# Performance work log

Measured on AMD Instinct MI355X. Metric: run time of the kernel, lower is better.

The kernel has to match this reference:

```python
import jax, jax.numpy as jnp
import numpy as np

B, C, H, W = 8, 64, 256, 256  # H must equal W (matmul shape constraint in original)


def setup_inputs() -> dict:
    key = jax.random.key(0)
    ks = jax.random.split(key, 7)
    s = 1.0 / np.sqrt(C)  # fan-in scaled init, like conv default scale
    return {
        "x": jax.random.normal(ks[0], (B, C, H, W), dtype=jnp.float32),
        "Wq": jax.random.normal(ks[1], (C, C), dtype=jnp.float32) * s,
        "bq": jax.random.normal(ks[2], (C,), dtype=jnp.float32) * s,
        "Wk": jax.random.normal(ks[3], (C, C), dtype=jnp.float32) * s,
        "bk": jax.random.normal(ks[4], (C,), dtype=jnp.float32) * s,
        "Wv": jax.random.normal(ks[5], (C, C), dtype=jnp.float32) * s,
        "bv": jax.random.normal(ks[6], (C,), dtype=jnp.float32) * s,
    }


def _conv1x1(x, Wt, b):
    # 1x1 Conv2d == per-pixel GEMM over channels: [o,c] x [b,c,h,w] -> [b,o,h,w]
    return jnp.einsum("oc,bchw->bohw", Wt, x) + b[None, :, None, None]


def reference(x, Wq, bq, Wk, bk, Wv, bv):
    q = _conv1x1(x, Wq, bq)
    k = _conv1x1(x, Wk, bk)
    v = _conv1x1(x, Wv, bv)
    # attn[b,c,i,j] = sum_h q[b,c,h,i] * k[b,c,h,j]   (q^T @ k over spatial)
    attn = jnp.einsum("bchi,bchj->bcij", q, k)
    # softmax over the CHANNEL axis (dim=-3 in torch == axis 1 here)
    attn = jax.nn.softmax(attn, axis=1)
    # out[b,c,i,j] = sum_m attn[b,c,i,m] * v[b,c,m,j]  (requires H == W)
    out = jnp.einsum("bcim,bcmj->bcij", attn, v)
    return out
```

## Files before the change

kernel.cpp:

```cpp
#include <hip/hip_runtime.h>
#include <math.h>

constexpr int CH  = 64;
constexpr int WW  = 256;
constexpr int HWS = WW * WW;
constexpr int NB  = 8;

typedef __attribute__((ext_vector_type(8))) short bf16x8;
typedef __attribute__((ext_vector_type(4))) float f32x4;

__device__ inline ushort f2bf(float f) {
    uint u = __float_as_uint(f);
    u += 0x7fffu + ((u >> 16) & 1u);
    return (ushort)(u >> 16);
}

union FragU { uint u[4]; bf16x8 v; };

__global__ __launch_bounds__(256) void qkv_mfma(
    const float* __restrict__ x,
    const float* __restrict__ Wq, const float* __restrict__ bq,
    const float* __restrict__ Wk, const float* __restrict__ bk,
    const float* __restrict__ Wv, const float* __restrict__ bv,
    float* __restrict__ Q, float* __restrict__ K, ushort* __restrict__ V)
{
    __shared__ ushort Xhi[128 * 64] __attribute__((aligned(16)));
    __shared__ ushort Xlo[128 * 64] __attribute__((aligned(16)));

    const int tid  = threadIdx.x;
    const int ln   = tid & 63;
    const int wid  = tid >> 6;
    const int ml   = ln & 15;
    const int quad = ln >> 4;

    const int n0 = blockIdx.x * 128;
    const int b  = n0 >> 16;
    const int pb = n0 & 65535;
    const float* xb = x + ((size_t)(b * CH) << 16);

    bf16x8 Ah[3][2], Al[3][2];
    float biasv[3][4];
#pragma unroll
    for (int a = 0; a < 3; ++a) {
        const int mt = wid * 3 + a;
        const float* Wsrc = (mt < 4) ? Wq : (mt < 8) ? Wk : Wv;
        const float* bsrc = (mt < 4) ? bq : (mt < 8) ? bk : bv;
        const int o = (mt & 3) * 16 + ml;
#pragma unroll
        for (int kf = 0; kf < 2; ++kf) {
            FragU Hh, Ll;
#pragma unroll
            for (int rp = 0; rp < 4; ++rp) {
                const float f0 = Wsrc[o * 64 + kf * 32 + quad * 8 + rp * 2];
                const float f1 = Wsrc[o * 64 + kf * 32 + quad * 8 + rp * 2 + 1];
                const uint u0 = __float_as_uint(f0);
                const uint u1 = __float_as_uint(f1);
                const float g0 = f0 - __uint_as_float(u0 & 0xffff0000u);
                const float g1 = f1 - __uint_as_float(u1 & 0xffff0000u);
                Hh.u[rp] = __builtin_amdgcn_perm(u1, u0, 0x07060302u);
                Ll.u[rp] = __builtin_amdgcn_perm(__float_as_uint(g1),
                                                 __float_as_uint(g0), 0x07060302u);
            }
            Ah[a][kf] = Hh.v; Al[a][kf] = Ll.v;
        }
#pragma unroll
        for (int r = 0; r < 4; ++r)
            biasv[a][r] = bsrc[(mt & 3) * 16 + quad * 4 + r];
    }

#pragma unroll
    for (int p = 0; p < 8; ++p) {
        const int flat = p * 256 + tid;
        const int c    = flat >> 5;
        const int px4  = (flat & 31) * 4;
        const float4 xv = *(const float4*)&xb[((size_t)c << 16) + pb + px4];
#pragma unroll
        for (int u = 0; u < 4; ++u) {
            const int px = px4 + u;
            const float f = (&xv.x)[u];
            const uint fu = __float_as_uint(f);
            const float lo = f - __uint_as_float(fu & 0xffff0000u);
            const int adr = px * 64 + ((((c >> 3) ^ ((px >> 1) & 7))) << 3) + (c & 7);
            Xhi[adr] = (ushort)(fu >> 16);
            Xlo[adr] = (ushort)(__float_as_uint(lo) >> 16);
        }
    }
    __syncthreads();

    f32x4 acc[3][8];
    const f32x4 zero = {0.f, 0.f, 0.f, 0.f};
#pragma unroll
    for (int a = 0; a < 3; ++a)
#pragma unroll
        for (int t = 0; t < 8; ++t) acc[a][t] = zero;

#pragma unroll
    for (int t = 0; t < 8; ++t) {
        const int px = t * 16 + ml;
        bf16x8 Bh[2], Bl[2];
#pragma unroll
        for (int kf = 0; kf < 2; ++kf) {
            const int g   = kf * 4 + quad;
            const int adr = px * 64 + ((g ^ ((px >> 1) & 7)) << 3);
            Bh[kf] = *(const bf16x8*)&Xhi[adr];
            Bl[kf] = *(const bf16x8*)&Xlo[adr];
        }
#pragma unroll
        for (int a = 0; a < 3; ++a) {
#pragma unroll
            for (int kf = 0; kf < 2; ++kf) {
                acc[a][t] = __builtin_amdgcn_mfma_f32_16x16x32_bf16(Ah[a][kf], Bh[kf], acc[a][t], 0, 0, 0);
                acc[a][t] = __builtin_amdgcn_mfma_f32_16x16x32_bf16(Ah[a][kf], Bl[kf], acc[a][t], 0, 0, 0);
                acc[a][t] = __builtin_amdgcn_mfma_f32_16x16x32_bf16(Al[a][kf], Bh[kf], acc[a][t], 0, 0, 0);
            }
        }
    }

#pragma unroll
    for (int a = 0; a < 3; ++a) {
        const int mt = wid * 3 + a;
        const int ch = (mt & 3) * 16 + quad * 4;
        if (mt < 4) {
#pragma unroll
            for (int t = 0; t < 8; ++t)
#pragma unroll
                for (int r = 0; r < 4; ++r)
                    Q[((size_t)(b * CH + ch + r) << 16) + pb + t * 16 + ml] =
                        acc[a][t][r] + biasv[a][r];
        } else if (mt < 8) {
#pragma unroll
            for (int t = 0; t < 8; ++t)
#pragma unroll
                for (int r = 0; r < 4; ++r)
                    K[((size_t)(b * CH + ch + r) << 16) + pb + t * 16 + ml] =
                        acc[a][t][r] + biasv[a][r];
        } else {
#pragma unroll
            for (int t = 0; t < 8; ++t)
#pragma unroll
                for (int r = 0; r < 4; ++r)
                    V[((size_t)(b * CH + ch + r) << 16) + pb + t * 16 + ml] =
                        f2bf(acc[a][t][r] + biasv[a][r]);
        }
    }
}

__device__ inline void frag_split(const float* __restrict__ S, int col, int quad,
                                  bf16x8* hi, bf16x8* lo) {
    FragU H, L;
#pragma unroll
    for (int rp = 0; rp < 4; ++rp) {
        const int h0 = quad * 8 + rp * 2;
        const int sw = ((h0 >> 1) & 7) << 2;
        const int c  = col ^ sw;
        const float f0 = S[(h0    ) * 128 + c];
        const float f1 = S[(h0 + 1) * 128 + c];
        const uint u0 = __float_as_uint(f0);
        const uint u1 = __float_as_uint(f1);
        const float g0 = f0 - __uint_as_float(u0 & 0xffff0000u);
        const float g1 = f1 - __uint_as_float(u1 & 0xffff0000u);
        H.u[rp] = __builtin_amdgcn_perm(u1, u0, 0x07060302u);
        L.u[rp] = __builtin_amdgcn_perm(__float_as_uint(g1), __float_as_uint(g0),
                                        0x07060302u);
    }
    *hi = H.v; *lo = L.v;
}

__global__ __launch_bounds__(256, 3) void attn_mfma(
    const float* __restrict__ Q, const float* __restrict__ Kt,
    float* __restrict__ attn)
{
    const int gid = blockIdx.x;
    const int bc  = gid >> 2;
    const int i0  = ((gid >> 1) & 1) * 128;
    const int j0  = (gid & 1) * 128;
    const float* q = Q  + (size_t)bc * HWS;
    const float* k = Kt + (size_t)bc * HWS;
    float* out     = attn + (size_t)bc * HWS;

    __shared__ float As[32 * 128];
    __shared__ float Bs[32 * 128];

    const int tid  = threadIdx.x;
    const int L    = tid & 63;
    const int wid  = tid >> 6;
    const int wy   = (wid >> 1) * 64;
    const int wx   = (wid & 1) * 64;
    const int ml   = L & 15;
    const int quad = L >> 4;

    f32x4 zero = {0.f, 0.f, 0.f, 0.f};
    f32x4 acc[4][4];
#pragma unroll
    for (int a = 0; a < 4; ++a)
#pragma unroll
        for (int b = 0; b < 4; ++b) acc[a][b] = zero;

    for (int k0 = 0; k0 < WW; k0 += 32) {
#pragma unroll
        for (int p = 0; p < 4; ++p) {
            const int flat = p * 256 + tid;
            const int hh   = flat >> 5;
            const int i4   = (flat & 31) * 4;
            const int sw   = ((hh >> 1) & 7) << 2;
            *(float4*)&As[hh * 128 + (i4 ^ sw)] =
                *(const float4*)&q[(size_t)(k0 + hh) * WW + i0 + i4];
            *(float4*)&Bs[hh * 128 + (i4 ^ sw)] =
                *(const float4*)&k[(size_t)(k0 + hh) * WW + j0 + i4];
        }
        __syncthreads();

        bf16x8 bh[4], bl[4];
#pragma unroll
        for (int t = 0; t < 4; ++t)
            frag_split(Bs, wx + t * 16 + ml, quad, &bh[t], &bl[t]);
#pragma unroll
        for (int a = 0; a < 4; ++a) {
            bf16x8 ah, al;
            frag_split(As, wy + a * 16 + ml, quad, &ah, &al);
#pragma unroll
            for (int b = 0; b < 4; ++b) {
                acc[a][b] = __builtin_amdgcn_mfma_f32_16x16x32_bf16(ah, bh[b], acc[a][b], 0, 0, 0);
                acc[a][b] = __builtin_amdgcn_mfma_f32_16x16x32_bf16(ah, bl[b], acc[a][b], 0, 0, 0);
                acc[a][b] = __builtin_amdgcn_mfma_f32_16x16x32_bf16(al, bh[b], acc[a][b], 0, 0, 0);
            }
        }
        __syncthreads();
    }

#pragma unroll
    for (int a = 0; a < 4; ++a)
#pragma unroll
        for (int b = 0; b < 4; ++b)
#pragma unroll
            for (int r = 0; r < 4; ++r)
                out[(size_t)(i0 + wy + a * 16 + quad * 4 + r) * WW
                    + j0 + wx + b * 16 + ml] = acc[a][b][r];
}

__global__ __launch_bounds__(256) void transpose_v(
    const ushort* __restrict__ Vb, ushort* __restrict__ Vt)
{
    const int blk = blockIdx.x;
    const int bc  = blk >> 2;
    const int m0  = ((blk >> 1) & 1) * 128;
    const int j0  = (blk & 1) * 128;
    const ushort* src = Vb + (size_t)bc * HWS;
    ushort* dst       = Vt + (size_t)bc * HWS;

    __shared__ ushort T[128][128] __attribute__((aligned(16)));

    const int tid = threadIdx.x;
#pragma unroll
    for (int p = 0; p < 8; ++p) {
        const int id  = p * 256 + tid;
        const int mm  = id >> 4;
        const int c16 = id & 15;
        const int cg  = (c16 + (mm >> 3)) & 15;
        *(uint4*)&T[mm][cg * 8] =
            *(const uint4*)(src + (size_t)(m0 + mm) * WW + j0 + c16 * 8);
    }
    __syncthreads();
#pragma unroll
    for (int p = 0; p < 4; ++p) {
        const int id  = p * 256 + tid;
        const int c16 = id & 15;
        const int jjp = id >> 4;
        const int jj  = jjp * 2;
        const int jjg = jj >> 3;
        ushort ra[8], rb[8];
#pragma unroll
        for (int u = 0; u < 8; ++u) {
            const int mm = c16 * 8 + u;
            const int cg = (jjg + c16) & 15;
            const uint pr = *(const uint*)&T[mm][cg * 8 + (jj & 7)];
            ra[u] = (ushort)(pr & 0xffffu);
            rb[u] = (ushort)(pr >> 16);
        }
        *(uint4*)(dst + (size_t)(j0 + jj)     * WW + m0 + c16 * 8) = *(uint4*)ra;
        *(uint4*)(dst + (size_t)(j0 + jj + 1) * WW + m0 + c16 * 8) = *(uint4*)rb;
    }
}

__global__ __launch_bounds__(128) void softmax_kernel(
    const float* __restrict__ logits, ushort* __restrict__ Wb)
{
    const int gid = blockIdx.x;
    const int b   = gid >> 8;
    const int i   = gid & 255;
    const int j2  = threadIdx.x * 2;
    const size_t off = (((size_t)(b * CH)) << 16) + (size_t)i * WW + j2;
    const float* base = logits + off;
    ushort* wout      = Wb + off;

    float2 v[CH];
#pragma unroll
    for (int c = 0; c < CH; ++c) v[c] = *(const float2*)&base[((size_t)c) << 16];

    float mx = v[0].x, my = v[0].y;
#pragma unroll
    for (int c = 1; c < CH; ++c) { mx = fmaxf(mx, v[c].x); my = fmaxf(my, v[c].y); }

    float sx = 0.f, sy = 0.f;
#pragma unroll
    for (int c = 0; c < CH; ++c) {
        v[c].x = __expf(v[c].x - mx); sx += v[c].x;
        v[c].y = __expf(v[c].y - my); sy += v[c].y;
    }
    const float ix = 1.0f / sx, iy = 1.0f / sy;
#pragma unroll
    for (int c = 0; c < CH; ++c) {
        ushort2 o;
        o.x = f2bf(v[c].x * ix);
        o.y = f2bf(v[c].y * iy);
        *(ushort2*)&wout[((size_t)c) << 16] = o;
    }
}

__global__ __launch_bounds__(256) void pv_kernel2(
    const ushort* __restrict__ Wb, const ushort* __restrict__ Vt,
    float* __restrict__ out)
{
    const int blk = blockIdx.x;
    const int bc  = blk >> 2;
    const int i0  = ((blk >> 1) & 1) * 128;
    const int j0  = (blk & 1) * 128;
    const ushort* w  = Wb + (size_t)bc * HWS;
    const ushort* vt = Vt + (size_t)bc * HWS;
    float* o         = out + (size_t)bc * HWS;

    __shared__ ushort As[128][40] __attribute__((aligned(16)));
    __shared__ ushort Bs[128][40] __attribute__((aligned(16)));

    const int tid  = threadIdx.x;
    const int L    = tid & 63;
    const int wid  = tid >> 6;
    const int wy   = (wid >> 1) * 64;
    const int wx   = (wid & 1) * 64;
    const int ml   = L & 15;
    const int quad = L >> 4;

    f32x4 zero = {0.f, 0.f, 0.f, 0.f};
    f32x4 acc[4][4];
#pragma unroll
    for (int a = 0; a < 4; ++a)
#pragma unroll
        for (int b = 0; b < 4; ++b) acc[a][b] = zero;

    for (int m0 = 0; m0 < WW; m0 += 32) {
#pragma unroll
        for (int p = 0; p < 2; ++p) {
            const int id  = p * 256 + tid;
            const int row = id >> 2;
            const int c4  = id & 3;
            *(uint4*)&As[row][c4 * 8] =
                *(const uint4*)(w  + (size_t)(i0 + row) * WW + m0 + c4 * 8);
            *(uint4*)&Bs[row][c4 * 8] =
                *(const uint4*)(vt + (size_t)(j0 + row) * WW + m0 + c4 * 8);
        }
        __syncthreads();

        bf16x8 af[4], bfr[4];
#pragma unroll
        for (int t = 0; t < 4; ++t)
            af[t]  = *(const bf16x8*)&As[wy + t * 16 + ml][quad * 8];
#pragma unroll
        for (int t = 0; t < 4; ++t)
            bfr[t] = *(const bf16x8*)&Bs[wx + t * 16 + ml][quad * 8];
#pragma unroll
        for (int a = 0; a < 4; ++a)
#pragma unroll
            for (int b = 0; b < 4; ++b)
                acc[a][b] = __builtin_amdgcn_mfma_f32_16x16x32_bf16(
                    af[a], bfr[b], acc[a][b], 0, 0, 0);
        __syncthreads();
    }

#pragma unroll
    for (int a = 0; a < 4; ++a)
#pragma unroll
        for (int b = 0; b < 4; ++b)
#pragma unroll
            for (int r = 0; r < 4; ++r)
                o[(size_t)(i0 + wy + a * 16 + quad * 4 + r) * WW
                  + j0 + wx + b * 16 + ml] = acc[a][b][r];
}

extern "C" void kernel_launch(void* const* d_in, const int* in_sizes, int n_in,
                              void* d_out, int out_size, void* d_ws, size_t ws_size,
                              hipStream_t stream) {
    const float* x  = (const float*)d_in[0];
    const float* Wq = (const float*)d_in[1];
    const float* bq = (const float*)d_in[2];
    const float* Wk = (const float*)d_in[3];
    const float* bk = (const float*)d_in[4];
    const float* Wv = (const float*)d_in[5];
    const float* bv = (const float*)d_in[6];
    float* out = (float*)d_out;

    const size_t NEL = (size_t)NB * CH * HWS;
    float*  Q  = (float*)d_ws;
    float*  K  = Q + NEL;
    ushort* Vb = (ushort*)(K + NEL);
    ushort* Vt = Vb + NEL;
    ushort* Wb = (ushort*)d_ws;

    qkv_mfma<<<(NB * HWS) / 128, 256, 0, stream>>>(x, Wq, bq, Wk, bk, Wv, bv, Q, K, Vb);
    attn_mfma<<<NB * CH * 4, 256, 0, stream>>>(Q, K, out);
    transpose_v<<<NB * CH * 4, 256, 0, stream>>>(Vb, Vt);
    softmax_kernel<<<NB * WW, 128, 0, stream>>>(out, Wb);
    pv_kernel2<<<NB * CH * 4, 256, 0, stream>>>(Wb, Vt, out);
}
```

Baseline: 615.3 us.

## Pre-pack Q/K as bf16 hi/lo pairs and load MFMA fragments directly from global

The QKV projection now stores Q and K as packed 32-bit words holding a bf16 high part and a bf16 residual, so the attention kernel no longer has to do the split arithmetic. The attention kernel drops the LDS staging, the barriers and the per-tile hi/lo split. Each lane gathers its fragment elements straight from global memory with strided scalar loads and assembles the hi and lo fragments with byte perms. This trades LDS traffic and synchronisation for uncoalesced-looking per-lane global loads (rows strided by WW) and more registers, and it removes the occupancy hint of 3 from launch bounds.

```diff
diff --git a/kernel.cpp b/kernel.cpp
--- a/kernel.cpp
+++ b/kernel.cpp
@@ -13,6 +13,12 @@
     uint u = __float_as_uint(f);
     u += 0x7fffu + ((u >> 16) & 1u);
     return (ushort)(u >> 16);
+}
+
+__device__ inline uint packsplit(float f) {
+    const uint fu = __float_as_uint(f);
+    const float lo = f - __uint_as_float(fu & 0xffff0000u);
+    return (fu & 0xffff0000u) | (__float_as_uint(lo) >> 16);
 }
 
 union FragU { uint u[4]; bf16x8 v; };
@@ -22,7 +28,7 @@
     const float* __restrict__ Wq, const float* __restrict__ bq,
     const float* __restrict__ Wk, const float* __restrict__ bk,
     const float* __restrict__ Wv, const float* __restrict__ bv,
-    float* __restrict__ Q, float* __restrict__ K, ushort* __restrict__ V)
+    uint* __restrict__ Q, uint* __restrict__ K, ushort* __restrict__ V)
 {
     __shared__ ushort Xhi[128 * 64] __attribute__((aligned(16)));
     __shared__ ushort Xlo[128 * 64] __attribute__((aligned(16)));
@@ -126,14 +132,14 @@
 #pragma unroll
                 for (int r = 0; r < 4; ++r)
                     Q[((size_t)(b * CH + ch + r) << 16) + pb + t * 16 + ml] =
-                        acc[a][t][r] + biasv[a][r];
+                        packsplit(acc[a][t][r] + biasv[a][r]);
         } else if (mt < 8) {
 #pragma unroll
             for (int t = 0; t < 8; ++t)
 #pragma unroll
                 for (int r = 0; r < 4; ++r)
                     K[((size_t)(b * CH + ch + r) << 16) + pb + t * 16 + ml] =
-                        acc[a][t][r] + biasv[a][r];
+                        packsplit(acc[a][t][r] + biasv[a][r]);
         } else {
 #pragma unroll
             for (int t = 0; t < 8; ++t)
@@ -145,41 +151,17 @@
     }
 }
 
-__device__ inline void frag_split(const float* __restrict__ S, int col, int quad,
-                                  bf16x8* hi, bf16x8* lo) {
-    FragU H, L;
-#pragma unroll
-    for (int rp = 0; rp < 4; ++rp) {
-        const int h0 = quad * 8 + rp * 2;
-        const int sw = ((h0 >> 1) & 7) << 2;
-        const int c  = col ^ sw;
-        const float f0 = S[(h0    ) * 128 + c];
-        const float f1 = S[(h0 + 1) * 128 + c];
-        const uint u0 = __float_as_uint(f0);
-        const uint u1 = __float_as_uint(f1);
-        const float g0 = f0 - __uint_as_float(u0 & 0xffff0000u);
-        const float g1 = f1 - __uint_as_float(u1 & 0xffff0000u);
-        H.u[rp] = __builtin_amdgcn_perm(u1, u0, 0x07060302u);
-        L.u[rp] = __builtin_amdgcn_perm(__float_as_uint(g1), __float_as_uint(g0),
-                                        0x07060302u);
-    }
-    *hi = H.v; *lo = L.v;
-}
-
-__global__ __launch_bounds__(256, 3) void attn_mfma(
-    const float* __restrict__ Q, const float* __restrict__ Kt,
+__global__ __launch_bounds__(256) void attn_mfma2(
+    const uint* __restrict__ Qp, const uint* __restrict__ Kp,
     float* __restrict__ attn)
 {
     const int gid = blockIdx.x;
     const int bc  = gid >> 2;
     const int i0  = ((gid >> 1) & 1) * 128;
     const int j0  = (gid & 1) * 128;
-    const float* q = Q  + (size_t)bc * HWS;
-    const float* k = Kt + (size_t)bc * HWS;
-    float* out     = attn + (size_t)bc * HWS;
-
-    __shared__ float As[32 * 128];
-    __shared__ float Bs[32 * 128];
+    const uint* q = Qp + (size_t)bc * HWS;
+    const uint* k = Kp + (size_t)bc * HWS;
+    float* out    = attn + (size_t)bc * HWS;
 
     const int tid  = threadIdx.x;
     const int L    = tid & 63;
@@ -189,7 +171,7 @@
     const int ml   = L & 15;
     const int quad = L >> 4;
 
-    f32x4 zero = {0.f, 0.f, 0.f, 0.f};
+    const f32x4 zero = {0.f, 0.f, 0.f, 0.f};
     f32x4 acc[4][4];
 #pragma unroll
     for (int a = 0; a < 4; ++a)
@@ -197,35 +179,51 @@
         for (int b = 0; b < 4; ++b) acc[a][b] = zero;
 
     for (int k0 = 0; k0 < WW; k0 += 32) {
-#pragma unroll
-        for (int p = 0; p < 4; ++p) {
-            const int flat = p * 256 + tid;
-            const int hh   = flat >> 5;
-            const int i4   = (flat & 31) * 4;
-            const int sw   = ((hh >> 1) & 7) << 2;
-            *(float4*)&As[hh * 128 + (i4 ^ sw)] =
-                *(const float4*)&q[(size_t)(k0 + hh) * WW + i0 + i4];
-            *(float4*)&Bs[hh * 128 + (i4 ^ sw)] =
-                *(const float4*)&k[(size_t)(k0 + hh) * WW + j0 + i4];
-        }
-        __syncthreads();
-
-        bf16x8 bh[4], bl[4];
-#pragma unroll
-        for (int t = 0; t < 4; ++t)
-            frag_split(Bs, wx + t * 16 + ml, quad, &bh[t], &bl[t]);
+        const size_t rb = (size_t)(k0 + quad * 8) * WW;
+        uint ua[4][8], ub[4][8];
 #pragma unroll
         for (int a = 0; a < 4; ++a) {
-            bf16x8 ah, al;
-            frag_split(As, wy + a * 16 + ml, quad, &ah, &al);
+            const uint* p = q + rb + i0 + wy + a * 16 + ml;
+#pragma unroll
+            for (int j = 0; j < 8; ++j) ua[a][j] = p[j * WW];
+        }
+#pragma unroll
+        for (int b = 0; b < 4; ++b) {
+            const uint* p = k + rb + j0 + wx + b * 16 + ml;
+#pragma unroll
+            for (int j = 0; j < 8; ++j) ub[b][j] = p[j * WW];
+        }
+
+        bf16x8 Ahf[4], Alf[4], Bhf[4], Blf[4];
+#pragma unroll
+        for (int a = 0; a < 4; ++a) {
+            FragU H, Lo;
+#pragma unroll
+            for (int rp = 0; rp < 4; ++rp) {
+                H.u[rp]  = __builtin_amdgcn_perm(ua[a][rp * 2 + 1], ua[a][rp * 2], 0x07060302u);
+                Lo.u[rp] = __builtin_amdgcn_perm(ua[a][rp * 2 + 1], ua[a][rp * 2], 0x05040100u);
+            }
+            Ahf[a] = H.v; Alf[a] = Lo.v;
+        }
+#pragma unroll
+        for (int b = 0; b < 4; ++b) {
+            FragU H, Lo;
+#pragma unroll
+            for (int rp = 0; rp < 4; ++rp) {
+                H.u[rp]  = __builtin_amdgcn_perm(ub[b][rp * 2 + 1], ub[b][rp * 2], 0x07060302u);
+                Lo.u[rp] = __builtin_amdgcn_perm(ub[b][rp * 2 + 1], ub[b][rp * 2], 0x05040100u);
+            }
+            Bhf[b] = H.v; Blf[b] = Lo.v;
+        }
+
+#pragma unroll
+        for (int a = 0; a < 4; ++a)
 #pragma unroll
             for (int b = 0; b < 4; ++b) {
-                acc[a][b] = __builtin_amdgcn_mfma_f32_16x16x32_bf16(ah, bh[b], acc[a][b], 0, 0, 0);
-                acc[a][b] = __builtin_amdgcn_mfma_f32_16x16x32_bf16(ah, bl[b], acc[a][b], 0, 0, 0);
-                acc[a][b] = __builtin_amdgcn_mfma_f32_16x16x32_bf16(al, bh[b], acc[a][b], 0, 0, 0);
+                acc[a][b] = __builtin_amdgcn_mfma_f32_16x16x32_bf16(Ahf[a], Bhf[b], acc[a][b], 0, 0, 0);
+                acc[a][b] = __builtin_amdgcn_mfma_f32_16x16x32_bf16(Ahf[a], Blf[b], acc[a][b], 0, 0, 0);
+                acc[a][b] = __builtin_amdgcn_mfma_f32_16x16x32_bf16(Alf[a], Bhf[b], acc[a][b], 0, 0, 0);
             }
-        }
-        __syncthreads();
     }
 
 #pragma unroll
@@ -399,14 +397,14 @@
     float* out = (float*)d_out;
 
     const size_t NEL = (size_t)NB * CH * HWS;
-    float*  Q  = (float*)d_ws;
-    float*  K  = Q + NEL;
-    ushort* Vb = (ushort*)(K + NEL);
+    uint*   Qp = (uint*)d_ws;
+    uint*   Kp = Qp + NEL;
+    ushort* Vb = (ushort*)(Kp + NEL);
     ushort* Vt = Vb + NEL;
     ushort* Wb = (ushort*)d_ws;
 
-    qkv_mfma<<<(NB * HWS) / 128, 256, 0, stream>>>(x, Wq, bq, Wk, bk, Wv, bv, Q, K, Vb);
-    attn_mfma<<<NB * CH * 4, 256, 0, stream>>>(Q, K, out);
+    qkv_mfma<<<(NB * HWS) / 128, 256, 0, stream>>>(x, Wq, bq, Wk, bk, Wv, bv, Qp, Kp, Vb);
+    attn_mfma2<<<NB * CH * 4, 256, 0, stream>>>(Qp, Kp, out);
     transpose_v<<<NB * CH * 4, 256, 0, stream>>>(Vb, Vt);
     softmax_kernel<<<NB * WW, 128, 0, stream>>>(out, Wb);
     pv_kernel2<<<NB * CH * 4, 256, 0, stream>>>(Wb, Vt, out);
```

After: 566.4 us. -8.0%, faster.
